# Kernel tuning notes

Measured on AMD Instinct MI355X. Metric: run time of the kernel, lower is better.

Reference implementation:

```python
import jax, jax.numpy as jnp
import numpy as np

N_NODES = 100000
NEG_SLOPE = 0.2  # PyG GATConv default


def gat_conv(x, src, dst, W, a_src, a_dst, n_nodes):
    """One PyG-style GATConv (with self-loops already appended to src/dst).
    x: [N, Fin], W: [Fin, H*C], a_src/a_dst: [H, C]. Returns [N, H, C]."""
    H, C = a_src.shape
    h = (x @ W).reshape(-1, H, C)                      # [N, H, C]
    s_src = jnp.einsum('nhc,hc->nh', h, a_src)         # [N, H]
    s_dst = jnp.einsum('nhc,hc->nh', h, a_dst)         # [N, H]
    e = jax.nn.leaky_relu(s_src[src] + s_dst[dst], NEG_SLOPE)  # [E, H]
    # segment softmax over incoming edges of each destination node
    e_max = jax.ops.segment_max(e, dst, num_segments=n_nodes)  # [N, H]
    e_exp = jnp.exp(e - e_max[dst])
    denom = jax.ops.segment_sum(e_exp, dst, num_segments=n_nodes)
    alpha = e_exp / (denom[dst] + 1e-16)               # [E, H]
    msg = h[src] * alpha[:, :, None]                   # [E, H, C]
    return jax.ops.segment_sum(msg, dst, num_segments=n_nodes)  # [N, H, C]


def setup_inputs() -> dict:
    key = jax.random.key(0)
    ks = jax.random.split(key, 10)
    in_dim, hidden, heads, out_dim = 128, 32, 4, 32
    N, E = N_NODES, 1600000
    x = jax.random.normal(ks[0], (N, in_dim), dtype=jnp.float32)
    edge_index = jax.random.randint(ks[1], (2, E), 0, N, dtype=jnp.int64)
    s = 0.1
    return {
        'x': x,
        'edge_index': edge_index,
        'W1': s * jax.random.normal(ks[2], (in_dim, heads * hidden), dtype=jnp.float32),
        'a_src1': s * jax.random.normal(ks[3], (heads, hidden), dtype=jnp.float32),
        'a_dst1': s * jax.random.normal(ks[4], (heads, hidden), dtype=jnp.float32),
        'b1': jnp.zeros((heads * hidden,), dtype=jnp.float32),
        'W2': s * jax.random.normal(ks[5], (heads * hidden, out_dim), dtype=jnp.float32),
        'a_src2': s * jax.random.normal(ks[6], (1, out_dim), dtype=jnp.float32),
        'a_dst2': s * jax.random.normal(ks[7], (1, out_dim), dtype=jnp.float32),
        'b2': jnp.zeros((out_dim,), dtype=jnp.float32),
    }


def reference(x, edge_index, W1, a_src1, a_dst1, b1, W2, a_src2, a_dst2, b2):
    N = x.shape[0]
    loops = jnp.arange(N, dtype=edge_index.dtype)
    src = jnp.concatenate([edge_index[0], loops])  # PyG adds self-loops
    dst = jnp.concatenate([edge_index[1], loops])
    h1 = gat_conv(x, src, dst, W1, a_src1, a_dst1, N)      # [N, H, C]
    h1 = jax.nn.elu(h1.reshape(N, -1) + b1)                # concat heads + bias, elu
    h2 = gat_conv(h1, src, dst, W2, a_src2, a_dst2, N)     # [N, 1, out]
    return h2.mean(axis=1) + b2                            # concat=False -> mean over heads
```

## Files before the change

### kernel.cpp

```cpp
#include <hip/hip_runtime.h>
#include <hip/hip_bf16.h>

#define NEG 0.2f
#define BK_SHIFT 9
#define BK_CAP 9216

typedef short short8 __attribute__((ext_vector_type(8)));
typedef float f32x4 __attribute__((ext_vector_type(4)));

__device__ __forceinline__ float lrelu(float x){ return x > 0.f ? x : NEG * x; }
__device__ __forceinline__ float elu_f(float x){ return x > 0.f ? x : expm1f(x); }
__device__ __forceinline__ unsigned short f2bf(float f){
  unsigned int u = __float_as_uint(f);
  unsigned int r = u + 0x7fffu + ((u >> 16) & 1u);
  return (unsigned short)(r >> 16);
}
__device__ __forceinline__ float bf2f(unsigned short u){
  return __uint_as_float(((unsigned int)u) << 16);
}

__global__ __launch_bounds__(512) void k_binA(
    const int* __restrict__ src, const int* __restrict__ dst, int E,
    int* __restrict__ gcursor, int2* __restrict__ ebuf){
  __shared__ int hist[256];
  __shared__ int base[256];
  int t = threadIdx.x;
  if (t < 256) hist[t] = 0;
  __syncthreads();
  int e0 = blockIdx.x * 4096;
  for (int j = 0; j < 8; j++){
    int e = e0 + j * 512 + t;
    if (e < E) atomicAdd(&hist[dst[e] >> BK_SHIFT], 1);
  }
  __syncthreads();
  if (t < 256){
    int cnt = hist[t];
    if (cnt > 0) base[t] = atomicAdd(&gcursor[t], cnt);
    hist[t] = 0;
  }
  __syncthreads();
  for (int j = 0; j < 8; j++){
    int e = e0 + j * 512 + t;
    if (e < E){
      int d = dst[e]; int b = d >> BK_SHIFT;
      int loc = atomicAdd(&hist[b], 1);
      ebuf[(size_t)b * BK_CAP + base[b] + loc] = make_int2(src[e], d);
    }
  }
}

__global__ __launch_bounds__(1024) void k_csrC(
    const int2* __restrict__ ebuf, const int* __restrict__ gcount,
    int* __restrict__ rowp, int* __restrict__ csr, int N, int NBK, int total){
  __shared__ int hist[512];
  __shared__ int psum[256];
  __shared__ int bsum[256];
  int b = blockIdx.x, t = threadIdx.x;
  int nbase = b << BK_SHIFT;
  int cnt = gcount[b];
  const int2* eb = ebuf + (size_t)b * BK_CAP;
  if (t < 512) hist[t] = 0;
  int bv = 0;
  if (t < 256){
    int nodes = 0;
    if (t < NBK){ int nb = N - (t << BK_SHIFT); nodes = nb > 512 ? 512 : nb; bv = gcount[t] + nodes; }
    bsum[t] = bv;
  }
  __syncthreads();
  for (int off = 1; off < 256; off <<= 1){
    int x = (t >= off && t < 256) ? bsum[t - off] : 0;
    __syncthreads();
    if (t < 256) bsum[t] += x;
    __syncthreads();
  }
  for (int i = t; i < cnt; i += 1024)
    atomicAdd(&hist[eb[i].y - nbase], 1);
  __syncthreads();
  int v0 = 0, v1 = 0, ps = 0;
  if (t < 256){ v0 = hist[2 * t]; v1 = hist[2 * t + 1]; ps = v0 + v1; psum[t] = ps; }
  __syncthreads();
  for (int off = 1; off < 256; off <<= 1){
    int x = (t >= off && t < 256) ? psum[t - off] : 0;
    __syncthreads();
    if (t < 256) psum[t] += x;
    __syncthreads();
  }
  if (t < 256){
    int eo = psum[t] - ps;
    int bb = (b == 0) ? 0 : bsum[b - 1];
    int n0 = 2 * t, n1 = 2 * t + 1;
    int r0 = bb + eo + n0;
    int r1 = bb + eo + v0 + n1;
    if (nbase + n0 < N) rowp[nbase + n0] = r0;
    if (nbase + n1 < N) rowp[nbase + n1] = r1;
    hist[n0] = r0; hist[n1] = r1;
  }
  if (b == 0 && t == 0) rowp[N] = total;
  __syncthreads();
  for (int i = t; i < cnt; i += 1024){
    int2 e = eb[i];
    int pos = atomicAdd(&hist[e.y - nbase], 1);
    csr[pos] = e.x;
  }
  __syncthreads();
  if (t < 256){
    int n0 = 2 * t, n1 = 2 * t + 1;
    if (nbase + n0 < N) csr[hist[n0]] = nbase + n0;
    if (nbase + n1 < N) csr[hist[n1]] = nbase + n1;
  }
}

__global__ __launch_bounds__(128) void k_packW(
    const float* __restrict__ W, unsigned short* __restrict__ Wp){
  int n = blockIdx.x, k = threadIdx.x;
  Wp[n * 128 + k] = f2bf(W[(size_t)k * 128 + n]);
}

__global__ __launch_bounds__(256, 3) void k_gemm1(
    const float* __restrict__ x, const unsigned short* __restrict__ Wp,
    const float* __restrict__ a_src, const float* __restrict__ a_dst,
    unsigned short* __restrict__ h_bf, float* __restrict__ ss, float* __restrict__ sd, int N){
  __shared__ unsigned short Wt[128 * 136];
  __shared__ unsigned short Xb[64 * 136];
  int t = threadIdx.x;
  int rb = blockIdx.x * 64;

  #pragma unroll
  for (int j = 0; j < 8; j++){
    int fi = j * 256 + t;
    int n = fi >> 4, ch = fi & 15;
    *(uint4*)&Wt[n * 136 + ch * 8] = *(const uint4*)&Wp[n * 128 + ch * 8];
  }
  #pragma unroll
  for (int j = 0; j < 8; j++){
    int fi = j * 256 + t;
    int row = fi >> 5, k4 = (fi & 31) * 4;
    int gr = rb + row;
    float4 v = make_float4(0.f, 0.f, 0.f, 0.f);
    if (gr < N) v = *(const float4*)&x[(size_t)gr * 128 + k4];
    uint2 pk;
    pk.x = ((unsigned)f2bf(v.y) << 16) | f2bf(v.x);
    pk.y = ((unsigned)f2bf(v.w) << 16) | f2bf(v.z);
    *(uint2*)&Xb[row * 136 + k4] = pk;
  }
  __syncthreads();

  int w = t >> 6, l = t & 63;
  int m = l & 15, quad = l >> 4;
  f32x4 acc[8];
  #pragma unroll
  for (int ct = 0; ct < 8; ct++) acc[ct] = (f32x4){0.f, 0.f, 0.f, 0.f};

  #pragma unroll
  for (int kc = 0; kc < 4; kc++){
    short8 a = *(const short8*)&Xb[(w * 16 + m) * 136 + kc * 32 + quad * 8];
    #pragma unroll
    for (int ct = 0; ct < 8; ct++){
      short8 b = *(const short8*)&Wt[(ct * 16 + m) * 136 + kc * 32 + quad * 8];
      acc[ct] = __builtin_amdgcn_mfma_f32_16x16x32_bf16(a, b, acc[ct], 0, 0, 0);
    }
  }

  float as[8], ad[8];
  #pragma unroll
  for (int ct = 0; ct < 8; ct++){ as[ct] = a_src[ct * 16 + m]; ad[ct] = a_dst[ct * 16 + m]; }

  #pragma unroll
  for (int reg = 0; reg < 4; reg++){
    int gr = rb + w * 16 + quad * 4 + reg;
    bool ok = gr < N;
    if (ok){
      #pragma unroll
      for (int ct = 0; ct < 8; ct++)
        h_bf[(size_t)gr * 128 + ct * 16 + m] = f2bf(acc[ct][reg]);
    }
    #pragma unroll
    for (int hh = 0; hh < 4; hh++){
      float ps = acc[2*hh][reg] * as[2*hh] + acc[2*hh+1][reg] * as[2*hh+1];
      float pd = acc[2*hh][reg] * ad[2*hh] + acc[2*hh+1][reg] * ad[2*hh+1];
      ps += __shfl_xor(ps, 1, 16); ps += __shfl_xor(ps, 2, 16);
      ps += __shfl_xor(ps, 4, 16); ps += __shfl_xor(ps, 8, 16);
      pd += __shfl_xor(pd, 1, 16); pd += __shfl_xor(pd, 2, 16);
      pd += __shfl_xor(pd, 4, 16); pd += __shfl_xor(pd, 8, 16);
      if (m == 0 && ok){ ss[(size_t)gr * 4 + hh] = ps; sd[(size_t)gr * 4 + hh] = pd; }
    }
  }
}

__global__ __launch_bounds__(256) void k_agg1(
    const int* __restrict__ row_ptr, const int* __restrict__ csr_src,
    const float* __restrict__ ss, const float* __restrict__ sdst,
    const __hip_bfloat162* __restrict__ hb2,
    unsigned int* __restrict__ out1_bf, int N){
  int n = blockIdx.x * 4 + (threadIdx.x >> 6);
  if (n >= N) return;
  int l = threadIdx.x & 63;
  int hd = l >> 4;
  float sdv = sdst[(size_t)n * 4 + hd];
  int j8 = l & 7, hh8 = (l >> 3) & 3;
  float sw8 = sdst[(size_t)n * 4 + hh8];
  int j4 = l & 3, hh4 = (l >> 2) & 3;
  float sw4 = sdst[(size_t)n * 4 + hh4];
  int beg = row_ptr[n], end = row_ptr[n + 1];
  float ax = 0.f, ay = 0.f, sw = 0.f;
  int e = beg;
  for (; e + 8 <= end; e += 8){
    int sj = csr_src[e + j8];
    float wv = __expf(lrelu(ss[(size_t)sj * 4 + hh8] + sw8));
    int s0 = __shfl(sj, 0, 8), s1 = __shfl(sj, 1, 8), s2 = __shfl(sj, 2, 8), s3 = __shfl(sj, 3, 8);
    int s4 = __shfl(sj, 4, 8), s5 = __shfl(sj, 5, 8), s6 = __shfl(sj, 6, 8), s7 = __shfl(sj, 7, 8);
    float w0 = __shfl(wv, hd * 8 + 0, 32), w1 = __shfl(wv, hd * 8 + 1, 32);
    float w2 = __shfl(wv, hd * 8 + 2, 32), w3 = __shfl(wv, hd * 8 + 3, 32);
    float w4 = __shfl(wv, hd * 8 + 4, 32), w5 = __shfl(wv, hd * 8 + 5, 32);
    float w6 = __shfl(wv, hd * 8 + 6, 32), w7 = __shfl(wv, hd * 8 + 7, 32);
    float2 v0 = __bfloat1622float2(hb2[(size_t)s0 * 64 + l]);
    float2 v1 = __bfloat1622float2(hb2[(size_t)s1 * 64 + l]);
    float2 v2 = __bfloat1622float2(hb2[(size_t)s2 * 64 + l]);
    float2 v3 = __bfloat1622float2(hb2[(size_t)s3 * 64 + l]);
    float2 v4 = __bfloat1622float2(hb2[(size_t)s4 * 64 + l]);
    float2 v5 = __bfloat1622float2(hb2[(size_t)s5 * 64 + l]);
    float2 v6 = __bfloat1622float2(hb2[(size_t)s6 * 64 + l]);
    float2 v7 = __bfloat1622float2(hb2[(size_t)s7 * 64 + l]);
    ax += w0*v0.x + w1*v1.x + w2*v2.x + w3*v3.x + w4*v4.x + w5*v5.x + w6*v6.x + w7*v7.x;
    ay += w0*v0.y + w1*v1.y + w2*v2.y + w3*v3.y + w4*v4.y + w5*v5.y + w6*v6.y + w7*v7.y;
    sw += w0 + w1 + w2 + w3 + w4 + w5 + w6 + w7;
  }
  for (; e + 4 <= end; e += 4){
    int sj = csr_src[e + j4];
    float wv = __expf(lrelu(ss[(size_t)sj * 4 + hh4] + sw4));
    int s0 = __shfl(sj, 0, 4), s1 = __shfl(sj, 1, 4);
    int s2 = __shfl(sj, 2, 4), s3 = __shfl(sj, 3, 4);
    float w0 = __shfl(wv, hd * 4 + 0, 16), w1 = __shfl(wv, hd * 4 + 1, 16);
    float w2 = __shfl(wv, hd * 4 + 2, 16), w3 = __shfl(wv, hd * 4 + 3, 16);
    float2 v0 = __bfloat1622float2(hb2[(size_t)s0 * 64 + l]);
    float2 v1 = __bfloat1622float2(hb2[(size_t)s1 * 64 + l]);
    float2 v2 = __bfloat1622float2(hb2[(size_t)s2 * 64 + l]);
    float2 v3 = __bfloat1622float2(hb2[(size_t)s3 * 64 + l]);
    ax += w0*v0.x + w1*v1.x + w2*v2.x + w3*v3.x;
    ay += w0*v0.y + w1*v1.y + w2*v2.y + w3*v3.y;
    sw += w0 + w1 + w2 + w3;
  }
  for (; e < end; e++){
    int s = csr_src[e];
    float w = __expf(lrelu(ss[(size_t)s * 4 + hd] + sdv));
    float2 v = __bfloat1622float2(hb2[(size_t)s * 64 + l]);
    ax += w*v.x; ay += w*v.y; sw += w;
  }
  float inv = 1.f / (sw + 1e-16f);
  unsigned int lo = f2bf(ax * inv), hi = f2bf(ay * inv);
  out1_bf[(size_t)n * 64 + l] = (hi << 16) | lo;
}

__global__ __launch_bounds__(256) void k_gemm2(
    const unsigned int* __restrict__ out1_bf, const float* __restrict__ b1,
    const float* __restrict__ W2,
    const float* __restrict__ a_src, const float* __restrict__ a_dst,
    unsigned short* __restrict__ h2_bf, float* __restrict__ s_src2, float* __restrict__ s_dst2, int N){
  __shared__ __align__(16) float Wl[128 * 32];
  __shared__ __align__(16) float Xl[64 * 132];
  int t = threadIdx.x;
  int rb = blockIdx.x * 64;

  const float4* Wg4 = (const float4*)W2;
  float4* Wl4 = (float4*)Wl;
  #pragma unroll
  for (int j = 0; j < 4; j++) Wl4[j * 256 + t] = Wg4[j * 256 + t];

  #pragma unroll
  for (int j = 0; j < 4; j++){
    int fi = j * 256 + t;
    int row = fi >> 4, q = fi & 15;
    int gr = rb + row;
    float v[8] = {0.f,0.f,0.f,0.f,0.f,0.f,0.f,0.f};
    if (gr < N){
      uint4 u = *(const uint4*)&out1_bf[(size_t)gr * 64 + q * 4];
      float4 bva = *(const float4*)&b1[q * 8];
      float4 bvb = *(const float4*)&b1[q * 8 + 4];
      v[0] = elu_f(bf2f((unsigned short)(u.x & 0xffff)) + bva.x);
      v[1] = elu_f(bf2f((unsigned short)(u.x >> 16))    + bva.y);
      v[2] = elu_f(bf2f((unsigned short)(u.y & 0xffff)) + bva.z);
      v[3] = elu_f(bf2f((unsigned short)(u.y >> 16))    + bva.w);
      v[4] = elu_f(bf2f((unsigned short)(u.z & 0xffff)) + bvb.x);
      v[5] = elu_f(bf2f((unsigned short)(u.z >> 16))    + bvb.y);
      v[6] = elu_f(bf2f((unsigned short)(u.w & 0xffff)) + bvb.z);
      v[7] = elu_f(bf2f((unsigned short)(u.w >> 16))    + bvb.w);
    }
    #pragma unroll
    for (int i = 0; i < 8; i++) Xl[row * 132 + q * 8 + i] = v[i];
  }
  __syncthreads();

  int cg = t & 7, rg = t >> 3;
  int c0 = cg * 4, r0 = rg * 2;
  float acc[2][4] = {};

  #pragma unroll 8
  for (int k = 0; k < 128; k++){
    float a0 = Xl[r0 * 132 + k];
    float a1 = Xl[(r0 + 1) * 132 + k];
    float4 b = *(float4*)&Wl[k * 32 + c0];
    acc[0][0] += a0 * b.x; acc[0][1] += a0 * b.y; acc[0][2] += a0 * b.z; acc[0][3] += a0 * b.w;
    acc[1][0] += a1 * b.x; acc[1][1] += a1 * b.y; acc[1][2] += a1 * b.z; acc[1][3] += a1 * b.w;
  }

  float as[4], ad[4];
  #pragma unroll
  for (int j = 0; j < 4; j++){ as[j] = a_src[c0 + j]; ad[j] = a_dst[c0 + j]; }
  #pragma unroll
  for (int i = 0; i < 2; i++){
    int row = rb + r0 + i;
    if (row < N){
      ushort4 o;
      o.x = f2bf(acc[i][0]); o.y = f2bf(acc[i][1]); o.z = f2bf(acc[i][2]); o.w = f2bf(acc[i][3]);
      *(ushort4*)&h2_bf[(size_t)row * 32 + c0] = o;
    }
    float ps = 0.f, pd = 0.f;
    #pragma unroll
    for (int j = 0; j < 4; j++){ ps += acc[i][j] * as[j]; pd += acc[i][j] * ad[j]; }
    ps += __shfl_xor(ps, 1, 8); ps += __shfl_xor(ps, 2, 8); ps += __shfl_xor(ps, 4, 8);
    pd += __shfl_xor(pd, 1, 8); pd += __shfl_xor(pd, 2, 8); pd += __shfl_xor(pd, 4, 8);
    if ((t & 7) == 0 && row < N){ s_src2[row] = ps; s_dst2[row] = pd; }
  }
}

__global__ __launch_bounds__(256) void k_agg2(
    const int* __restrict__ row_ptr, const int* __restrict__ csr_src,
    const float* __restrict__ ss2, const float* __restrict__ sd2,
    const unsigned short* __restrict__ h2bf, const float* __restrict__ b2,
    float* __restrict__ out, int N){
  int n = blockIdx.x * 8 + (threadIdx.x >> 5);
  if (n >= N) return;
  int c = threadIdx.x & 31;
  float sdv = sd2[n];
  int beg = row_ptr[n], end = row_ptr[n + 1];
  float acc = 0.f, sw = 0.f;
  int e = beg;
  int j8 = c & 7;
  for (; e + 8 <= end; e += 8){
    int sj = csr_src[e + j8];
    float wv = __expf(lrelu(ss2[sj] + sdv));
    int s0 = __shfl(sj, 0, 8), s1 = __shfl(sj, 1, 8), s2 = __shfl(sj, 2, 8), s3 = __shfl(sj, 3, 8);
    int s4 = __shfl(sj, 4, 8), s5 = __shfl(sj, 5, 8), s6 = __shfl(sj, 6, 8), s7 = __shfl(sj, 7, 8);
    float w0 = __shfl(wv, 0, 8), w1 = __shfl(wv, 1, 8), w2 = __shfl(wv, 2, 8), w3 = __shfl(wv, 3, 8);
    float w4 = __shfl(wv, 4, 8), w5 = __shfl(wv, 5, 8), w6 = __shfl(wv, 6, 8), w7 = __shfl(wv, 7, 8);
    float v0 = bf2f(h2bf[(size_t)s0 * 32 + c]);
    float v1 = bf2f(h2bf[(size_t)s1 * 32 + c]);
    float v2 = bf2f(h2bf[(size_t)s2 * 32 + c]);
    float v3 = bf2f(h2bf[(size_t)s3 * 32 + c]);
    float v4 = bf2f(h2bf[(size_t)s4 * 32 + c]);
    float v5 = bf2f(h2bf[(size_t)s5 * 32 + c]);
    float v6 = bf2f(h2bf[(size_t)s6 * 32 + c]);
    float v7 = bf2f(h2bf[(size_t)s7 * 32 + c]);
    acc += w0*v0 + w1*v1 + w2*v2 + w3*v3 + w4*v4 + w5*v5 + w6*v6 + w7*v7;
    sw += w0 + w1 + w2 + w3 + w4 + w5 + w6 + w7;
  }
  for (; e + 4 <= end; e += 4){
    int s0 = csr_src[e], s1 = csr_src[e+1], s2 = csr_src[e+2], s3 = csr_src[e+3];
    int sj = csr_src[e + (c & 3)];
    float wv = __expf(lrelu(ss2[sj] + sdv));
    float w0 = __shfl(wv, 0, 4), w1 = __shfl(wv, 1, 4);
    float w2 = __shfl(wv, 2, 4), w3 = __shfl(wv, 3, 4);
    float v0 = bf2f(h2bf[(size_t)s0 * 32 + c]);
    float v1 = bf2f(h2bf[(size_t)s1 * 32 + c]);
    float v2 = bf2f(h2bf[(size_t)s2 * 32 + c]);
    float v3 = bf2f(h2bf[(size_t)s3 * 32 + c]);
    acc += w0*v0 + w1*v1 + w2*v2 + w3*v3;
    sw += w0 + w1 + w2 + w3;
  }
  for (; e < end; e++){
    int s = csr_src[e];
    float w = __expf(lrelu(ss2[s] + sdv));
    acc += w * bf2f(h2bf[(size_t)s * 32 + c]);
    sw += w;
  }
  out[(size_t)n * 32 + c] = acc / (sw + 1e-16f) + b2[c];
}

extern "C" void kernel_launch(void* const* d_in, const int* in_sizes, int n_in,
                              void* d_out, int out_size, void* d_ws, size_t ws_size,
                              hipStream_t stream) {
  const float* x      = (const float*)d_in[0];
  const int*   ei     = (const int*)  d_in[1];
  const float* W1     = (const float*)d_in[2];
  const float* a_src1 = (const float*)d_in[3];
  const float* a_dst1 = (const float*)d_in[4];
  const float* b1     = (const float*)d_in[5];
  const float* W2     = (const float*)d_in[6];
  const float* a_src2 = (const float*)d_in[7];
  const float* a_dst2 = (const float*)d_in[8];
  const float* b2     = (const float*)d_in[9];
  float* out = (float*)d_out;

  int N = in_sizes[0] / 128;
  int E = in_sizes[1] / 2;
  const int* srcp = ei;
  const int* dstp = ei + E;
  int total = E + N;
  int NBK = (N + 511) >> 9;

  char* p = (char*)d_ws;
  auto alloc = [&](size_t bytes) -> void* {
    void* r = (void*)p; p += (bytes + 255) & ~(size_t)255; return r;
  };
  unsigned short* h_bf    = (unsigned short*)alloc((size_t)N * 128 * 2);
  unsigned int*   out1_bf = (unsigned int*)alloc((size_t)N * 64 * 4);
  unsigned short* h2_bf   = (unsigned short*)alloc((size_t)N * 32 * 2);
  unsigned short* Wp      = (unsigned short*)alloc(128 * 128 * 2);
  float* ss1  = (float*)alloc((size_t)N * 4 * 4);
  float* sd1  = (float*)alloc((size_t)N * 4 * 4);
  float* ss2  = (float*)alloc((size_t)N * 4);
  float* sd2  = (float*)alloc((size_t)N * 4);
  int* rowp   = (int*)alloc((size_t)(N + 1) * 4);
  int* csr    = (int*)alloc((size_t)total * 4);
  int* gcur   = (int*)alloc(256 * 4);
  int2* ebuf  = (int2*)out1_bf;
  (void)ws_size; (void)n_in; (void)out_size;

  hipMemsetAsync(gcur, 0, 256 * 4, stream);
  k_binA<<<(E + 4095) / 4096, 512, 0, stream>>>(srcp, dstp, E, gcur, ebuf);
  k_csrC<<<NBK, 1024, 0, stream>>>(ebuf, gcur, rowp, csr, N, NBK, total);

  k_packW<<<128, 128, 0, stream>>>(W1, Wp);
  k_gemm1<<<(N + 63) / 64, 256, 0, stream>>>(x, Wp, a_src1, a_dst1, h_bf, ss1, sd1, N);
  k_agg1<<<(N + 3) / 4, 256, 0, stream>>>(rowp, csr, ss1, sd1, (const __hip_bfloat162*)h_bf, out1_bf, N);
  k_gemm2<<<(N + 63) / 64, 256, 0, stream>>>(out1_bf, b1, W2, a_src2, a_dst2, h2_bf, ss2, sd2, N);
  k_agg2<<<(N + 7) / 8, 256, 0, stream>>>(rowp, csr, ss2, sd2, h2_bf, b2, out, N);
}
```

Before: 309.1 us.

## Restructure aggregation kernels to gather multiple edges per wave with wide loads

Both aggregation kernels now process 16 edges per iteration. Each wave's lanes are split into slots that gather different source rows at once using 16-byte (layer 1) or 8-byte (layer 2) vector loads, instead of one 4- or 2-byte element per lane per edge. The next chunk's indices and source scores are prefetched while the current chunk is accumulated. Partial sums are combined with cross-lane shuffles at the end. The aim is more memory parallelism and fewer load instructions in these gather-bound kernels, at the cost of more registers, a final reduction, and idle lanes on low-degree nodes.

```diff
diff --git a/kernel.cpp b/kernel.cpp
--- a/kernel.cpp
+++ b/kernel.cpp
@@ -17,6 +17,12 @@
 }
 __device__ __forceinline__ float bf2f(unsigned short u){
   return __uint_as_float(((unsigned int)u) << 16);
+}
+__device__ __forceinline__ float2 bfu2(unsigned int v){
+  float2 r;
+  r.x = __uint_as_float(v << 16);
+  r.y = __uint_as_float(v & 0xffff0000u);
+  return r;
 }
 
 __global__ __launch_bounds__(512) void k_binA(
@@ -190,65 +196,75 @@
 __global__ __launch_bounds__(256) void k_agg1(
     const int* __restrict__ row_ptr, const int* __restrict__ csr_src,
     const float* __restrict__ ss, const float* __restrict__ sdst,
-    const __hip_bfloat162* __restrict__ hb2,
+    const unsigned short* __restrict__ hb,
     unsigned int* __restrict__ out1_bf, int N){
   int n = blockIdx.x * 4 + (threadIdx.x >> 6);
   if (n >= N) return;
   int l = threadIdx.x & 63;
-  int hd = l >> 4;
-  float sdv = sdst[(size_t)n * 4 + hd];
-  int j8 = l & 7, hh8 = (l >> 3) & 3;
-  float sw8 = sdst[(size_t)n * 4 + hh8];
-  int j4 = l & 3, hh4 = (l >> 2) & 3;
-  float sw4 = sdst[(size_t)n * 4 + hh4];
+  int q  = (l & 7) + ((l >> 5) << 3);
+  int hh = (l >> 3) & 3;
+  int slot = l >> 4;
+  int c = l & 15;
+  int hd = c >> 2;
+  float sdw = sdst[(size_t)n * 4 + hh];
   int beg = row_ptr[n], end = row_ptr[n + 1];
-  float ax = 0.f, ay = 0.f, sw = 0.f;
+
+  float acc[8] = {0.f,0.f,0.f,0.f,0.f,0.f,0.f,0.f};
+  float swacc = 0.f;
+
   int e = beg;
-  for (; e + 8 <= end; e += 8){
-    int sj = csr_src[e + j8];
-    float wv = __expf(lrelu(ss[(size_t)sj * 4 + hh8] + sw8));
-    int s0 = __shfl(sj, 0, 8), s1 = __shfl(sj, 1, 8), s2 = __shfl(sj, 2, 8), s3 = __shfl(sj, 3, 8);
-    int s4 = __shfl(sj, 4, 8), s5 = __shfl(sj, 5, 8), s6 = __shfl(sj, 6, 8), s7 = __shfl(sj, 7, 8);
-    float w0 = __shfl(wv, hd * 8 + 0, 32), w1 = __shfl(wv, hd * 8 + 1, 32);
-    float w2 = __shfl(wv, hd * 8 + 2, 32), w3 = __shfl(wv, hd * 8 + 3, 32);
-    float w4 = __shfl(wv, hd * 8 + 4, 32), w5 = __shfl(wv, hd * 8 + 5, 32);
-    float w6 = __shfl(wv, hd * 8 + 6, 32), w7 = __shfl(wv, hd * 8 + 7, 32);
-    float2 v0 = __bfloat1622float2(hb2[(size_t)s0 * 64 + l]);
-    float2 v1 = __bfloat1622float2(hb2[(size_t)s1 * 64 + l]);
-    float2 v2 = __bfloat1622float2(hb2[(size_t)s2 * 64 + l]);
-    float2 v3 = __bfloat1622float2(hb2[(size_t)s3 * 64 + l]);
-    float2 v4 = __bfloat1622float2(hb2[(size_t)s4 * 64 + l]);
-    float2 v5 = __bfloat1622float2(hb2[(size_t)s5 * 64 + l]);
-    float2 v6 = __bfloat1622float2(hb2[(size_t)s6 * 64 + l]);
-    float2 v7 = __bfloat1622float2(hb2[(size_t)s7 * 64 + l]);
-    ax += w0*v0.x + w1*v1.x + w2*v2.x + w3*v3.x + w4*v4.x + w5*v5.x + w6*v6.x + w7*v7.x;
-    ay += w0*v0.y + w1*v1.y + w2*v2.y + w3*v3.y + w4*v4.y + w5*v5.y + w6*v6.y + w7*v7.y;
-    sw += w0 + w1 + w2 + w3 + w4 + w5 + w6 + w7;
-  }
-  for (; e + 4 <= end; e += 4){
-    int sj = csr_src[e + j4];
-    float wv = __expf(lrelu(ss[(size_t)sj * 4 + hh4] + sw4));
-    int s0 = __shfl(sj, 0, 4), s1 = __shfl(sj, 1, 4);
-    int s2 = __shfl(sj, 2, 4), s3 = __shfl(sj, 3, 4);
-    float w0 = __shfl(wv, hd * 4 + 0, 16), w1 = __shfl(wv, hd * 4 + 1, 16);
-    float w2 = __shfl(wv, hd * 4 + 2, 16), w3 = __shfl(wv, hd * 4 + 3, 16);
-    float2 v0 = __bfloat1622float2(hb2[(size_t)s0 * 64 + l]);
-    float2 v1 = __bfloat1622float2(hb2[(size_t)s1 * 64 + l]);
-    float2 v2 = __bfloat1622float2(hb2[(size_t)s2 * 64 + l]);
-    float2 v3 = __bfloat1622float2(hb2[(size_t)s3 * 64 + l]);
-    ax += w0*v0.x + w1*v1.x + w2*v2.x + w3*v3.x;
-    ay += w0*v0.y + w1*v1.y + w2*v2.y + w3*v3.y;
-    sw += w0 + w1 + w2 + w3;
-  }
-  for (; e < end; e++){
-    int s = csr_src[e];
-    float w = __expf(lrelu(ss[(size_t)s * 4 + hd] + sdv));
-    float2 v = __bfloat1622float2(hb2[(size_t)s * 64 + l]);
-    ax += w*v.x; ay += w*v.y; sw += w;
-  }
+  int remaining = end - beg;
+  int qc = q < remaining ? q : 0;
+  int sj = csr_src[e + qc];
+  float sv = ss[(size_t)sj * 4 + hh];
+
+  while (remaining > 0){
+    int cur = remaining > 16 ? 16 : remaining;
+    float wv = (q < cur) ? __expf(lrelu(sv + sdw)) : 0.f;
+    swacc += wv;
+    int sjc = sj;
+    int rn = remaining - 16;
+    if (rn > 0){
+      int qn = q < rn ? q : 0;
+      sj = csr_src[e + 16 + qn];
+      sv = ss[(size_t)sj * 4 + hh];
+    }
+    #pragma unroll
+    for (int p = 0; p < 4; p++){
+      if ((p << 2) < cur){
+        int sl = ((p & 1) << 2) + slot + ((p >> 1) << 5);
+        int s  = __shfl(sjc, sl, 64);
+        float w = __shfl(wv, sl + (hd << 3), 64);
+        uint4 u = *(const uint4*)&hb[(size_t)s * 128 + (c << 3)];
+        float2 f0 = bfu2(u.x), f1 = bfu2(u.y), f2 = bfu2(u.z), f3 = bfu2(u.w);
+        acc[0] += w * f0.x; acc[1] += w * f0.y;
+        acc[2] += w * f1.x; acc[3] += w * f1.y;
+        acc[4] += w * f2.x; acc[5] += w * f2.y;
+        acc[6] += w * f3.x; acc[7] += w * f3.y;
+      }
+    }
+    e += 16; remaining = rn;
+  }
+
+  #pragma unroll
+  for (int i = 0; i < 8; i++){
+    acc[i] += __shfl_xor(acc[i], 16, 64);
+    acc[i] += __shfl_xor(acc[i], 32, 64);
+  }
+  swacc += __shfl_xor(swacc, 1, 64);
+  swacc += __shfl_xor(swacc, 2, 64);
+  swacc += __shfl_xor(swacc, 4, 64);
+  swacc += __shfl_xor(swacc, 32, 64);
+  float sw = __shfl(swacc, hd << 3, 64);
   float inv = 1.f / (sw + 1e-16f);
-  unsigned int lo = f2bf(ax * inv), hi = f2bf(ay * inv);
-  out1_bf[(size_t)n * 64 + l] = (hi << 16) | lo;
+  if (slot == 0){
+    unsigned int o0 = ((unsigned)f2bf(acc[1] * inv) << 16) | f2bf(acc[0] * inv);
+    unsigned int o1 = ((unsigned)f2bf(acc[3] * inv) << 16) | f2bf(acc[2] * inv);
+    unsigned int o2 = ((unsigned)f2bf(acc[5] * inv) << 16) | f2bf(acc[4] * inv);
+    unsigned int o3 = ((unsigned)f2bf(acc[7] * inv) << 16) | f2bf(acc[6] * inv);
+    uint4 o; o.x = o0; o.y = o1; o.z = o2; o.w = o3;
+    *(uint4*)&out1_bf[(size_t)n * 64 + (c << 2)] = o;
+  }
 }
 
 __global__ __launch_bounds__(256) void k_gemm2(
@@ -328,52 +344,68 @@
     const float* __restrict__ ss2, const float* __restrict__ sd2,
     const unsigned short* __restrict__ h2bf, const float* __restrict__ b2,
     float* __restrict__ out, int N){
-  int n = blockIdx.x * 8 + (threadIdx.x >> 5);
+  int n = blockIdx.x * 4 + (threadIdx.x >> 6);
   if (n >= N) return;
-  int c = threadIdx.x & 31;
+  int l = threadIdx.x & 63;
+  int q = l & 15;
+  int slot = l >> 3;
+  int ch4 = l & 7;
   float sdv = sd2[n];
   int beg = row_ptr[n], end = row_ptr[n + 1];
-  float acc = 0.f, sw = 0.f;
+
+  float acc[4] = {0.f,0.f,0.f,0.f};
+  float swacc = 0.f;
+
   int e = beg;
-  int j8 = c & 7;
-  for (; e + 8 <= end; e += 8){
-    int sj = csr_src[e + j8];
-    float wv = __expf(lrelu(ss2[sj] + sdv));
-    int s0 = __shfl(sj, 0, 8), s1 = __shfl(sj, 1, 8), s2 = __shfl(sj, 2, 8), s3 = __shfl(sj, 3, 8);
-    int s4 = __shfl(sj, 4, 8), s5 = __shfl(sj, 5, 8), s6 = __shfl(sj, 6, 8), s7 = __shfl(sj, 7, 8);
-    float w0 = __shfl(wv, 0, 8), w1 = __shfl(wv, 1, 8), w2 = __shfl(wv, 2, 8), w3 = __shfl(wv, 3, 8);
-    float w4 = __shfl(wv, 4, 8), w5 = __shfl(wv, 5, 8), w6 = __shfl(wv, 6, 8), w7 = __shfl(wv, 7, 8);
-    float v0 = bf2f(h2bf[(size_t)s0 * 32 + c]);
-    float v1 = bf2f(h2bf[(size_t)s1 * 32 + c]);
-    float v2 = bf2f(h2bf[(size_t)s2 * 32 + c]);
-    float v3 = bf2f(h2bf[(size_t)s3 * 32 + c]);
-    float v4 = bf2f(h2bf[(size_t)s4 * 32 + c]);
-    float v5 = bf2f(h2bf[(size_t)s5 * 32 + c]);
-    float v6 = bf2f(h2bf[(size_t)s6 * 32 + c]);
-    float v7 = bf2f(h2bf[(size_t)s7 * 32 + c]);
-    acc += w0*v0 + w1*v1 + w2*v2 + w3*v3 + w4*v4 + w5*v5 + w6*v6 + w7*v7;
-    sw += w0 + w1 + w2 + w3 + w4 + w5 + w6 + w7;
-  }
-  for (; e + 4 <= end; e += 4){
-    int s0 = csr_src[e], s1 = csr_src[e+1], s2 = csr_src[e+2], s3 = csr_src[e+3];
-    int sj = csr_src[e + (c & 3)];
-    float wv = __expf(lrelu(ss2[sj] + sdv));
-    float w0 = __shfl(wv, 0, 4), w1 = __shfl(wv, 1, 4);
-    float w2 = __shfl(wv, 2, 4), w3 = __shfl(wv, 3, 4);
-    float v0 = bf2f(h2bf[(size_t)s0 * 32 + c]);
-    float v1 = bf2f(h2bf[(size_t)s1 * 32 + c]);
-    float v2 = bf2f(h2bf[(size_t)s2 * 32 + c]);
-    float v3 = bf2f(h2bf[(size_t)s3 * 32 + c]);
-    acc += w0*v0 + w1*v1 + w2*v2 + w3*v3;
-    sw += w0 + w1 + w2 + w3;
-  }
-  for (; e < end; e++){
-    int s = csr_src[e];
-    float w = __expf(lrelu(ss2[s] + sdv));
-    acc += w * bf2f(h2bf[(size_t)s * 32 + c]);
-    sw += w;
-  }
-  out[(size_t)n * 32 + c] = acc / (sw + 1e-16f) + b2[c];
+  int remaining = end - beg;
+  int qc = q < remaining ? q : 0;
+  int sj = csr_src[e + qc];
+  float sv = ss2[sj];
+
+  while (remaining > 0){
+    int cur = remaining > 16 ? 16 : remaining;
+    float wv = (q < cur) ? __expf(lrelu(sv + sdv)) : 0.f;
+    swacc += wv;
+    int sjc = sj;
+    int rn = remaining - 16;
+    if (rn > 0){
+      int qn = q < rn ? q : 0;
+      sj = csr_src[e + 16 + qn];
+      sv = ss2[sj];
+    }
+    #pragma unroll
+    for (int p = 0; p < 2; p++){
+      if ((p << 3) < cur){
+        int sl = (p << 3) + slot;
+        int s  = __shfl(sjc, sl, 64);
+        float w = __shfl(wv, sl, 64);
+        uint2 u = *(const uint2*)&h2bf[(size_t)s * 32 + (ch4 << 2)];
+        float2 f0 = bfu2(u.x), f1 = bfu2(u.y);
+        acc[0] += w * f0.x; acc[1] += w * f0.y;
+        acc[2] += w * f1.x; acc[3] += w * f1.y;
+      }
+    }
+    e += 16; remaining = rn;
+  }
+
+  #pragma unroll
+  for (int i = 0; i < 4; i++){
+    acc[i] += __shfl_xor(acc[i], 8, 64);
+    acc[i] += __shfl_xor(acc[i], 16, 64);
+    acc[i] += __shfl_xor(acc[i], 32, 64);
+  }
+  swacc += __shfl_xor(swacc, 1, 64);
+  swacc += __shfl_xor(swacc, 2, 64);
+  swacc += __shfl_xor(swacc, 4, 64);
+  swacc += __shfl_xor(swacc, 8, 64);
+  float inv = 1.f / (swacc + 1e-16f);
+  if (slot == 0){
+    float4 bv = *(const float4*)&b2[ch4 << 2];
+    float4 o;
+    o.x = acc[0] * inv + bv.x; o.y = acc[1] * inv + bv.y;
+    o.z = acc[2] * inv + bv.z; o.w = acc[3] * inv + bv.w;
+    *(float4*)&out[(size_t)n * 32 + (ch4 << 2)] = o;
+  }
 }
 
 extern "C" void kernel_launch(void* const* d_in, const int* in_sizes, int n_in,
@@ -422,7 +454,7 @@
 
   k_packW<<<128, 128, 0, stream>>>(W1, Wp);
   k_gemm1<<<(N + 63) / 64, 256, 0, stream>>>(x, Wp, a_src1, a_dst1, h_bf, ss1, sd1, N);
-  k_agg1<<<(N + 3) / 4, 256, 0, stream>>>(rowp, csr, ss1, sd1, (const __hip_bfloat162*)h_bf, out1_bf, N);
+  k_agg1<<<(N + 3) / 4, 256, 0, stream>>>(rowp, csr, ss1, sd1, h_bf, out1_bf, N);
   k_gemm2<<<(N + 63) / 64, 256, 0, stream>>>(out1_bf, b1, W2, a_src2, a_dst2, h2_bf, ss2, sd2, N);
-  k_agg2<<<(N + 7) / 8, 256, 0, stream>>>(rowp, csr, ss2, sd2, h2_bf, b2, out, N);
-}
+  k_agg2<<<(N + 3) / 4, 256, 0, stream>>>(rowp, csr, ss2, sd2, h2_bf, b2, out, N);
+}
```

Result: no change. 313.9 us (+1.5%).
